# Kernel optimization log

Hardware: AMD Instinct MI355X
Metric: run time of the kernel (lower is better)

Reference implementation:

```python
import jax, jax.numpy as jnp
import numpy as np

B, C, HH, WW = 256, 1024, 7, 7
S = HH * WW            # 49 tokens
D = 1024               # hidden_size
L = 2                  # encoder_layers (nhead arg, swapped in source)
H = 2                  # attention heads (num_layers arg, swapped in source)
HD = D // H            # 512 head dim
FF = 1024              # encoder_ffn_dim
OUT = 1024             # head output
EPS = 1e-5


def setup_inputs() -> dict:
    key = jax.random.key(0)
    ks = jax.random.split(key, 10)
    n = lambda k, shape: jax.random.normal(k, shape, jnp.float32) * 0.02
    return dict(
        x=jax.random.normal(ks[0], (B, C, HH, WW), jnp.float32),
        pos_emb=n(ks[1], (S, D)),
        ln1_s=jnp.ones((L, D), jnp.float32), ln1_b=jnp.zeros((L, D), jnp.float32),
        wq=n(ks[2], (L, D, D)), wk=n(ks[3], (L, D, D)),
        wv=n(ks[4], (L, D, D)), wo=n(ks[5], (L, D, D)),
        ln2_s=jnp.ones((L, D), jnp.float32), ln2_b=jnp.zeros((L, D), jnp.float32),
        w1=n(ks[6], (L, D, FF)), b1=jnp.zeros((L, FF), jnp.float32),
        w2=n(ks[7], (L, FF, D)), b2=jnp.zeros((L, D), jnp.float32),
        lnf_s=jnp.ones((D,), jnp.float32), lnf_b=jnp.zeros((D,), jnp.float32),
        head_w=n(ks[8], (S * D, OUT)), head_b=jnp.zeros((OUT,), jnp.float32),
    )


def _ln(x, s, b):
    m = jnp.mean(x, axis=-1, keepdims=True)
    v = jnp.var(x, axis=-1, keepdims=True)
    return (x - m) * jax.lax.rsqrt(v + EPS) * s + b


def reference(x, pos_emb, ln1_s, ln1_b, wq, wk, wv, wo, ln2_s, ln2_b,
              w1, b1, w2, b2, lnf_s, lnf_b, head_w, head_b):
    b = x.shape[0]
    # flatten HxW then permute -> [B, S, D] token sequence
    h = x.reshape(b, C, S).transpose(0, 2, 1)
    # BigBirdPegasus encoder: learned pos emb added to inputs_embeds (no scaling path)
    h = h + pos_emb[None, :, :]
    scale = 1.0 / jnp.sqrt(jnp.float32(HD))
    for i in range(L):
        # --- self-attention block (pre-LN); seq_len=49 triggers original_full attention ---
        r = h
        hn = _ln(h, ln1_s[i], ln1_b[i])
        q = (hn @ wq[i]).reshape(b, S, H, HD)
        k = (hn @ wk[i]).reshape(b, S, H, HD)
        v = (hn @ wv[i]).reshape(b, S, H, HD)
        scores = jnp.einsum('bqhd,bkhd->bhqk', q, k) * scale
        attn = jax.nn.softmax(scores, axis=-1)
        ctx = jnp.einsum('bhqk,bkhd->bqhd', attn, v).reshape(b, S, D)
        h = r + ctx @ wo[i]
        # --- feed-forward block (pre-LN, gelu_new) ---
        r = h
        hn = _ln(h, ln2_s[i], ln2_b[i])
        hn = jax.nn.gelu(hn @ w1[i] + b1[i], approximate=True)
        h = r + hn @ w2[i] + b2[i]
    # BigBirdPegasus applies layernorm_embedding AFTER the layer stack
    h = _ln(h, lnf_s, lnf_b)
    # flatten + linear + relu head
    out = jax.nn.relu(h.reshape(b, S * D) @ head_w + head_b)
    return out
```

## Files before the change

kernel.cpp:

```cpp
#include <hip/hip_runtime.h>
#include <hip/hip_bf16.h>
#include <stdint.h>

#define Bq 256
#define Sq 49
#define Dq 1024
#define Hq 2
#define HDq 512
#define Mq (Bq*Sq)
#define KHEADq (Sq*Dq)
#define STq 3072

typedef unsigned short u16;
typedef short bf16x8 __attribute__((ext_vector_type(8)));
typedef float f32x4 __attribute__((ext_vector_type(4)));

__device__ inline u16 f2bf(float f){
  union { float f; uint32_t u; } c; c.f = f;
  uint32_t r = c.u + 0x7FFFu + ((c.u >> 16) & 1u);
  return (u16)(r >> 16);
}
__device__ inline float bf2f(u16 h){
  union { uint32_t u; float f; } c; c.u = ((uint32_t)h) << 16;
  return c.f;
}

#define GLOAD_LDS16(gp, lp) \
  __builtin_amdgcn_global_load_lds((__attribute__((address_space(1))) void*)(gp), \
                                   (__attribute__((address_space(3))) void*)(lp), 16, 0, 0)
#define MFMA16(a,b,c) __builtin_amdgcn_mfma_f32_16x16x32_bf16(a,b,c,0,0,0)

__global__ __launch_bounds__(256) void prep_kernel(const float* __restrict__ x,
    const float* __restrict__ pos, u16* __restrict__ h, float2* __restrict__ pstat,
    u16* __restrict__ qkv){
  __shared__ float t[49*129];
  int b = blockIdx.x, c0 = blockIdx.y*128;
  int tid = threadIdx.x, lane = tid & 63, wave = tid >> 6;
  if(b == 0){
    uint4* pz = (uint4*)(qkv + (size_t)Mq*STq + (size_t)blockIdx.y*6144);
    pz[tid] = make_uint4(0,0,0,0);
    pz[256+tid] = make_uint4(0,0,0,0);
    pz[512+tid] = make_uint4(0,0,0,0);
  }
  const float* xb = x + (size_t)b*(Dq*Sq) + (size_t)c0*Sq;
  #pragma unroll
  for(int i=0;i<32;i++){
    int cc = wave + i*4;
    if(lane < Sq) t[lane*129 + cc] = xb[(size_t)cc*Sq + lane];
  }
  __syncthreads();
  #pragma unroll
  for(int p=0;p<25;p++){
    int idx = p*256 + tid;
    int s = idx >> 7, cc = idx & 127;
    if(s < Sq){
      float hv = t[s*129 + cc] + pos[s*Dq + c0 + cc];
      h[((size_t)b*Sq + s)*Dq + c0 + cc] = f2bf(hv);
      t[s*129 + cc] = hv;
    }
  }
  __syncthreads();
  int r = tid >> 2, qd = tid & 3;
  if(r < Sq){
    float S=0.f, Q=0.f;
    for(int cc=qd; cc<128; cc+=4){ float vv = t[r*129+cc]; S+=vv; Q+=vv*vv; }
    S += __shfl_xor(S,1); Q += __shfl_xor(Q,1);
    S += __shfl_xor(S,2); Q += __shfl_xor(Q,2);
    if(qd==0){ float2 pp; pp.x=S; pp.y=Q; pstat[(size_t)blockIdx.y*Mq + b*Sq + r] = pp; }
  }
}

__global__ __launch_bounds__(256) void ln_kernel(const u16* __restrict__ hin,
    const float* __restrict__ sc, const float* __restrict__ bi, u16* __restrict__ outp){
  int wave = threadIdx.x >> 6, lane = threadIdx.x & 63;
  int row = blockIdx.x*4 + wave;
  const u16* p = hin + (size_t)row*Dq + lane*16;
  uint4 t0 = *(const uint4*)p;
  uint4 t1 = *(const uint4*)(p + 8);
  float v[16];
  {
    uint32_t wds[8] = {t0.x,t0.y,t0.z,t0.w,t1.x,t1.y,t1.z,t1.w};
    #pragma unroll
    for(int i=0;i<8;i++){
      v[2*i]   = bf2f((u16)(wds[i] & 0xffff));
      v[2*i+1] = bf2f((u16)(wds[i] >> 16));
    }
  }
  float s=0.f, sq=0.f;
  #pragma unroll
  for(int i=0;i<16;i++){ s += v[i]; sq += v[i]*v[i]; }
  #pragma unroll
  for(int o=32;o>=1;o>>=1){ s += __shfl_xor(s,o); sq += __shfl_xor(sq,o); }
  float mean = s * (1.f/Dq);
  float var  = sq * (1.f/Dq) - mean*mean;
  float rs = rsqrtf(var + 1e-5f);
  int c0 = lane*16;
  uint32_t w[8];
  #pragma unroll
  for(int i=0;i<8;i++){
    u16 lo = f2bf((v[2*i]   - mean)*rs*sc[c0+2*i]   + bi[c0+2*i]);
    u16 hi = f2bf((v[2*i+1] - mean)*rs*sc[c0+2*i+1] + bi[c0+2*i+1]);
    w[i] = (uint32_t)lo | ((uint32_t)hi << 16);
  }
  uint4* ob = (uint4*)(outp + (size_t)row*Dq + c0);
  ob[0] = make_uint4(w[0],w[1],w[2],w[3]);
  ob[1] = make_uint4(w[4],w[5],w[6],w[7]);
}

__global__ void transp_all(const float* __restrict__ wq, const float* __restrict__ wk,
    const float* __restrict__ wv, const float* __restrict__ wo,
    const float* __restrict__ w1, const float* __restrict__ w2,
    const float* __restrict__ ln1s, const float* __restrict__ ln2s, u16* __restrict__ outp){
  __shared__ float t[32][33];
  int slot = blockIdx.z; int l = slot / 6, j = slot - l*6;
  const float* srcs[6] = {wq,wk,wv,wo,w1,w2};
  const float* in = srcs[j] + (size_t)l*Dq*Dq;
  const float* sc = (j<3) ? (ln1s + l*Dq) : (j==4 ? (ln2s + l*Dq) : nullptr);
  u16* o = outp + (size_t)slot*Dq*Dq;
  int k0 = blockIdx.x*32, n0 = blockIdx.y*32;
  int tx = threadIdx.x, ty = threadIdx.y;
  #pragma unroll
  for(int i=0;i<4;i++) t[ty+8*i][tx] = in[(size_t)(k0+ty+8*i)*Dq + n0+tx];
  __syncthreads();
  float sck = sc ? sc[k0+tx] : 1.f;
  #pragma unroll
  for(int i=0;i<4;i++) o[(size_t)(n0+ty+8*i)*Dq + k0+tx] = f2bf(t[tx][ty+8*i] * sck);
}

__global__ __launch_bounds__(256) void uv_all_kernel(const float* __restrict__ wq,
    const float* __restrict__ wk, const float* __restrict__ wv, const float* __restrict__ w1,
    const float* __restrict__ ln1s, const float* __restrict__ ln1b,
    const float* __restrict__ ln2s, const float* __restrict__ ln2b, float* __restrict__ uvbuf){
  __shared__ float2 red[8][32];
  int t = threadIdx.x;
  int colg = blockIdx.x*32 + (t & 31);
  int ks = t >> 5;
  int l = colg >> 12, col = colg & 4095;
  int j = col >> 10, n = col & 1023;
  const float* srcs[4] = {wq, wk, wv, w1};
  const float* src = srcs[j] + (size_t)l*Dq*Dq;
  const float* sc = (j<3 ? ln1s : ln2s) + l*Dq;
  const float* bi = (j<3 ? ln1b : ln2b) + l*Dq;
  float u=0.f, v=0.f;
  for(int k=ks*128;k<ks*128+128;k++){
    float val = src[(size_t)k*Dq + n];
    u += sc[k]*val; v += bi[k]*val;
  }
  float2 pp; pp.x=u; pp.y=v;
  red[ks][t&31] = pp;
  __syncthreads();
  if(t < 32){
    float U=0.f, V=0.f;
    #pragma unroll
    for(int s2=0;s2<8;s2++){ float2 q2 = red[s2][t]; U+=q2.x; V+=q2.y; }
    uvbuf[(size_t)(blockIdx.x*32 + t)*2]   = U;
    uvbuf[(size_t)(blockIdx.x*32 + t)*2+1] = V;
  }
}

template<int EPI>
__global__ __launch_bounds__(512, 2) void gemm_nt2(
    const u16* __restrict__ A, int lda,
    const u16* __restrict__ Bt, int ldb,
    void* __restrict__ Cout, const u16* __restrict__ resid,
    const float* __restrict__ bias, int ldc,
    const float2* __restrict__ pstat_in, int nchunk,
    const float* __restrict__ uvp, float2* __restrict__ pstat_out)
{
  __shared__ u16 lds[65536];
  int tid = threadIdx.x, lane = tid & 63;
  int wave = tid >> 6;
  int wm = wave >> 2, wn = wave & 3;
  int l15 = lane & 15, l4 = lane >> 4;
  int swz = (l15 & 7) << 4;

  int gx = gridDim.x, nwg = gx*gridDim.y;
  int orig = blockIdx.y*gx + blockIdx.x;
  int qq = nwg >> 3, rr = nwg & 7;
  int xcd = orig & 7, idx = orig >> 3;
  int wgid = (xcd < rr ? xcd*(qq+1) : rr*(qq+1) + (xcd-rr)*qq) + idx;
  int bx = wgid % gx, by = wgid / gx;
  int m0 = by*256, n0 = bx*256;

  int srow = tid >> 3, scolb = (tid & 7) * 16;
  int scolx = scolb ^ ((srow & 7) << 4);
  auto stage2 = [&](int d, int kt, int h){
    #pragma unroll
    for(int cc=0; cc<2; cc++){
      int c = 2*h + cc;
      if(c < 4){
        int row = c*64 + srow;
        const u16* src = A + (size_t)(m0+row)*lda + kt*64 + (scolx>>1);
        GLOAD_LDS16(src, &lds[d*16384 + c*4096 + tid*8]);
      } else {
        int c4 = c - 4;
        int row = c4*64 + srow;
        const u16* src = Bt + (size_t)(n0+row)*ldb + kt*64 + (scolx>>1);
        GLOAD_LDS16(src, &lds[32768 + d*16384 + c4*4096 + tid*8]);
      }
    }
  };
  auto rdA = [&](int d, int i, int s)->bf16x8{
    int row = wm*128 + i*16 + l15;
    int byt = row*128 + ((s*64 + l4*16) ^ swz);
    return *(const bf16x8*)((const char*)lds + d*32768 + byt);
  };
  auto rdB = [&](int d, int n, int s)->bf16x8{
    int row = wn*64 + n*16 + l15;
    int byt = row*128 + ((s*64 + l4*16) ^ swz);
    return *(const bf16x8*)((const char*)lds + 65536 + d*32768 + byt);
  };

  f32x4 acc[8][4] = {};

  #pragma unroll
  for(int h=0;h<4;h++) stage2(0, 0, h);

  for(int t=0; t<16; ++t){
    int d = t & 1;
    bf16x8 bfr[4][2];
    if(t < 15){
      stage2(d^1, t+1, 0);
      asm volatile("s_waitcnt vmcnt(2)" ::: "memory");
    } else {
      asm volatile("s_waitcnt vmcnt(0)" ::: "memory");
    }
    __builtin_amdgcn_sched_barrier(0);
    __builtin_amdgcn_s_barrier();
    bfr[0][0]=rdB(d,0,0); bfr[0][1]=rdB(d,0,1);
    bfr[1][0]=rdB(d,1,0); bfr[1][1]=rdB(d,1,1);
    bf16x8 a0s0=rdA(d,0,0), a0s1=rdA(d,0,1), a1s0=rdA(d,1,0), a1s1=rdA(d,1,1);
    __builtin_amdgcn_s_setprio(1);
    acc[0][0]=MFMA16(a0s0,bfr[0][0],acc[0][0]); acc[0][0]=MFMA16(a0s1,bfr[0][1],acc[0][0]);
    acc[0][1]=MFMA16(a0s0,bfr[1][0],acc[0][1]); acc[0][1]=MFMA16(a0s1,bfr[1][1],acc[0][1]);
    acc[1][0]=MFMA16(a1s0,bfr[0][0],acc[1][0]); acc[1][0]=MFMA16(a1s1,bfr[0][1],acc[1][0]);
    acc[1][1]=MFMA16(a1s0,bfr[1][0],acc[1][1]); acc[1][1]=MFMA16(a1s1,bfr[1][1],acc[1][1]);
    __builtin_amdgcn_s_setprio(0);
    __builtin_amdgcn_s_barrier();
    bfr[2][0]=rdB(d,2,0); bfr[2][1]=rdB(d,2,1);
    bfr[3][0]=rdB(d,3,0); bfr[3][1]=rdB(d,3,1);
    if(t < 15) stage2(d^1, t+1, 1);
    __builtin_amdgcn_s_barrier();
    __builtin_amdgcn_s_setprio(1);
    acc[0][2]=MFMA16(a0s0,bfr[2][0],acc[0][2]); acc[0][2]=MFMA16(a0s1,bfr[2][1],acc[0][2]);
    acc[0][3]=MFMA16(a0s0,bfr[3][0],acc[0][3]); acc[0][3]=MFMA16(a0s1,bfr[3][1],acc[0][3]);
    acc[1][2]=MFMA16(a1s0,bfr[2][0],acc[1][2]); acc[1][2]=MFMA16(a1s1,bfr[2][1],acc[1][2]);
    acc[1][3]=MFMA16(a1s0,bfr[3][0],acc[1][3]); acc[1][3]=MFMA16(a1s1,bfr[3][1],acc[1][3]);
    __builtin_amdgcn_s_setprio(0);
    __builtin_amdgcn_s_barrier();
    #pragma unroll
    for(int q=1;q<4;q++){
      bf16x8 c0s0=rdA(d,2*q,0), c0s1=rdA(d,2*q,1), c1s0=rdA(d,2*q+1,0), c1s1=rdA(d,2*q+1,1);
      if(t < 15 && q < 3) stage2(d^1, t+1, q+1);
      __builtin_amdgcn_s_barrier();
      __builtin_amdgcn_s_setprio(1);
      #pragma unroll
      for(int n=0;n<4;n++){
        acc[2*q][n]   = MFMA16(c0s0, bfr[n][0], acc[2*q][n]);
        acc[2*q][n]   = MFMA16(c0s1, bfr[n][1], acc[2*q][n]);
        acc[2*q+1][n] = MFMA16(c1s0, bfr[n][0], acc[2*q+1][n]);
        acc[2*q+1][n] = MFMA16(c1s1, bfr[n][1], acc[2*q+1][n]);
      }
      __builtin_amdgcn_s_setprio(0);
      __builtin_amdgcn_s_barrier();
    }
  }

  if constexpr (EPI == 1){
    float2* statsS = (float2*)((char*)lds + 49152);
    float* slotf = (float*)((char*)lds + wave*4096);
    float bv[4];
    #pragma unroll
    for(int n=0;n<4;n++) bv[n] = bias ? bias[n0 + wn*64 + n*16 + l15] : 0.f;
    #pragma unroll
    for(int i=0;i<8;i++){
      #pragma unroll
      for(int n=0;n<4;n++)
        #pragma unroll
        for(int r=0;r<4;r++)
          slotf[(l4*4+r)*64 + n*16 + l15] = acc[i][n][r] + bv[n];
      #pragma unroll
      for(int st=0;st<2;st++){
        int u = st*64 + lane;
        int row = u >> 3, c8 = (u & 7)*8;
        f32x4 lo = *(const f32x4*)&slotf[row*64 + c8];
        f32x4 hi = *(const f32x4*)&slotf[row*64 + c8 + 4];
        size_t o = (size_t)(m0 + wm*128 + i*16 + row)*ldc + n0 + wn*64 + c8;
        bf16x8 rb = *(const bf16x8*)(resid + o);
        bf16x8 ov; float fs=0.f, fq=0.f;
        #pragma unroll
        for(int j=0;j<4;j++){
          float a_ = lo[j] + bf2f((u16)rb[j]);
          float b_ = hi[j] + bf2f((u16)rb[4+j]);
          ov[j]   = (short)f2bf(a_);
          ov[4+j] = (short)f2bf(b_);
          fs += a_ + b_; fq += a_*a_ + b_*b_;
        }
        *(bf16x8*)((u16*)Cout + o) = ov;
        fs += __shfl_xor(fs,1); fq += __shfl_xor(fq,1);
        fs += __shfl_xor(fs,2); fq += __shfl_xor(fq,2);
        fs += __shfl_xor(fs,4); fq += __shfl_xor(fq,4);
        if((lane&7)==0){
          float2 pp; pp.x=fs; pp.y=fq;
          statsS[(wm*128 + i*16 + st*8 + (lane>>3))*4 + wn] = pp;
        }
      }
    }
    __syncthreads();
    if(tid < 256){
      float S=0.f, Q=0.f;
      #pragma unroll
      for(int w2_=0;w2_<4;w2_++){ float2 pp = statsS[tid*4+w2_]; S+=pp.x; Q+=pp.y; }
      float2 pp; pp.x=S; pp.y=Q;
      pstat_out[(size_t)bx*Mq + m0 + tid] = pp;
    }
  } else {
    float2* lstat = (float2*)((char*)lds + 49152);
    if(tid < 256){
      float S=0.f, Q=0.f;
      for(int c=0;c<nchunk;c++){ float2 pp = pstat_in[(size_t)c*Mq + m0 + tid]; S+=pp.x; Q+=pp.y; }
      float mean = S*(1.f/1024.f);
      float var  = Q*(1.f/1024.f) - mean*mean;
      float2 sm; sm.x = rsqrtf(var + 1e-5f); sm.y = mean;
      lstat[tid] = sm;
    }
    __syncthreads();
    u16* slot = (u16*)((char*)lds + wave*2048);
    float uvv[4][2], bv[4];
    #pragma unroll
    for(int n=0;n<4;n++){
      int ncol = n0 + wn*64 + n*16 + l15;
      float2 uv2 = ((const float2*)uvp)[ncol];
      uvv[n][0] = uv2.x; uvv[n][1] = uv2.y;
      if constexpr (EPI == 2) bv[n] = bias[ncol];
    }
    #pragma unroll
    for(int i=0;i<8;i++){
      #pragma unroll
      for(int n=0;n<4;n++)
        #pragma unroll
        for(int r=0;r<4;r++){
          float2 sm = lstat[wm*128 + i*16 + l4*4 + r];
          float va = sm.x*acc[i][n][r] - sm.x*sm.y*uvv[n][0] + uvv[n][1];
          u16 ov;
          if constexpr (EPI == 0){
            ov = f2bf(va);
          } else {
            float xg = va + bv[n];
            float tg = tanhf(0.79788456080286536f*(xg + 0.044715f*xg*xg*xg));
            ov = f2bf(0.5f*xg*(1.f+tg));
          }
          slot[(l4*4+r)*64 + n*16 + l15] = ov;
        }
      #pragma unroll
      for(int st=0;st<2;st++){
        int u = st*64 + lane;
        int row = u >> 3, c8 = (u & 7)*8;
        bf16x8 v8 = *(const bf16x8*)&slot[row*64 + c8];
        *(bf16x8*)((u16*)Cout + (size_t)(m0 + wm*128 + i*16 + row)*ldc + n0 + wn*64 + c8) = v8;
      }
    }
  }
}

__global__ __launch_bounds__(256) void gemm_head(
    const u16* __restrict__ A, const float* __restrict__ W,
    u16* __restrict__ parts)
{
  __shared__ u16 sA[256*32];
  int tid = threadIdx.x, lane = tid & 63;
  int wave = tid >> 6;
  int wm = wave >> 1, wn = wave & 1;
  int l15 = lane & 15, l4 = lane >> 4;
  int c = blockIdx.x, r = blockIdx.y;
  int nz = (c==0) ? 7 : 6;
  int bx = r / nz;
  if(bx >= 8) return;
  int z = c + 8*(r - bx*nz);
  int n0 = bx*128;
  f32x4 acc[8][4] = {};
  const float* wp = W + ((size_t)z*1024 + (size_t)l4*8)*1024 + n0 + wn*64 + l15;
  for(int kt=0;kt<32;kt++){
    #pragma unroll
    for(int cc=0;cc<4;cc++){
      int s2 = cc*256+tid;
      GLOAD_LDS16(A + (size_t)(s2>>2)*KHEADq + (size_t)z*1024 + kt*32 + (s2&3)*8, &sA[s2*8]);
    }
    bf16x8 bfr[4];
    #pragma unroll
    for(int f=0;f<4;f++){
      float wreg[8];
      #pragma unroll
      for(int jj=0;jj<8;jj++)
        wreg[jj] = wp[(size_t)(kt*32+jj)*1024 + f*16];
      bf16x8 bv;
      #pragma unroll
      for(int jj=0;jj<8;jj++)
        bv[jj] = __builtin_bit_cast(short, __float2bfloat16(wreg[jj]));
      bfr[f] = bv;
    }
    __syncthreads();
    bf16x8 af[8];
    #pragma unroll
    for(int i=0;i<8;i++)
      af[i] = *(const bf16x8*)&sA[(wm*128 + i*16 + l15)*32 + l4*8];
    #pragma unroll
    for(int i=0;i<8;i++)
      #pragma unroll
      for(int j=0;j<4;j++)
        acc[i][j] = MFMA16(af[i], bfr[j], acc[i][j]);
    __syncthreads();
  }
  u16* slot = &sA[wave*2048];
  u16* base = parts + (size_t)z*(Bq*1024);
  #pragma unroll
  for(int i=0;i<8;i++){
    #pragma unroll
    for(int j=0;j<4;j++)
      #pragma unroll
      for(int rr=0;rr<4;rr++)
        slot[(l4*4+rr)*64 + j*16 + l15] = f2bf(acc[i][j][rr]);
    #pragma unroll
    for(int st=0;st<2;st++){
      int u = st*64 + lane;
      int row = u >> 3, c8 = (u & 7)*8;
      bf16x8 v8 = *(const bf16x8*)&slot[row*64 + c8];
      *(bf16x8*)(base + (size_t)(wm*128 + i*16 + row)*1024 + n0 + wn*64 + c8) = v8;
    }
  }
}

__global__ __launch_bounds__(256) void attn_kernel(u16* __restrict__ qkv)
{
  __shared__ float sS[64][65];
  __shared__ u16 sP[64][64];
  int bh = blockIdx.x;
  int b = bh >> 1, h = bh & 1;
  int tid = threadIdx.x, lane = tid & 63, wave = tid >> 6;
  int l15 = lane & 15, l4 = lane >> 4;
  f32x4 zero4 = {0.f,0.f,0.f,0.f};
  bf16x8 zb = {0,0,0,0,0,0,0,0};
  f32x4 acc[4];
  #pragma unroll
  for(int i=0;i<4;i++) acc[i] = zero4;
  int srow = wave*16 + l15;
  const u16* qp = qkv + (size_t)(b*Sq + srow)*STq + h*HDq + l4*8;
  const u16* kbase = qkv + (size_t)b*Sq*STq + Dq + h*HDq + l4*8;
  for(int kt=0;kt<16;kt++){
    bf16x8 aq = (srow < Sq) ? *(const bf16x8*)(qp + kt*32) : zb;
    #pragma unroll
    for(int fn=0;fn<4;fn++){
      int s2 = fn*16 + l15;
      bf16x8 bk = (s2 < Sq) ? *(const bf16x8*)(kbase + (size_t)s2*STq + kt*32) : zb;
      acc[fn] = MFMA16(aq, bk, acc[fn]);
    }
  }
  const float scale = 0.04419417382415922f;
  #pragma unroll
  for(int fn=0;fn<4;fn++)
    #pragma unroll
    for(int r=0;r<4;r++)
      sS[wave*16 + l4*4 + r][fn*16 + l15] = acc[fn][r]*scale;
  __syncthreads();
  {
    int r = tid >> 2, qd = tid & 3;
    float mx = -1e30f;
    for(int j=qd;j<Sq;j+=4) mx = fmaxf(mx, sS[r][j]);
    mx = fmaxf(mx, __shfl_xor(mx,1));
    mx = fmaxf(mx, __shfl_xor(mx,2));
    float sum = 0.f;
    for(int j=qd;j<Sq;j+=4){ float e = __expf(sS[r][j]-mx); sS[r][j]=e; sum+=e; }
    sum += __shfl_xor(sum,1);
    sum += __shfl_xor(sum,2);
    float inv = 1.f/sum;
    for(int j=qd;j<64;j+=4) sP[r][j] = (j<Sq)? f2bf(sS[r][j]*inv) : (u16)0;
  }
  __syncthreads();
  bf16x8 ap[2];
  #pragma unroll
  for(int kt2=0;kt2<2;kt2++)
    ap[kt2] = *(const bf16x8*)&sP[wave*16 + l15][kt2*32 + l4*8];
  const u16* vbp = qkv + (size_t)b*Sq*STq + 2*Dq + h*HDq + l15;
  u16* cb = qkv + (size_t)b*Sq*STq + h*HDq;
  for(int fn=0;fn<32;fn++){
    f32x4 c4 = zero4;
    #pragma unroll
    for(int kt2=0;kt2<2;kt2++){
      const u16* vp = vbp + fn*16 + (size_t)(kt2*32 + l4*8)*STq;
      bf16x8 bv;
      #pragma unroll
      for(int jj=0;jj<8;jj++) bv[jj] = (short)vp[(size_t)jj*STq];
      c4 = MFMA16(ap[kt2], bv, c4);
    }
    #pragma unroll
    for(int r=0;r<4;r++){
      int s = wave*16 + l4*4 + r;
      if(s < Sq) cb[(size_t)s*STq + fn*16 + l15] = f2bf(c4[r]);
    }
  }
}

__global__ __launch_bounds__(256) void head_finalize(const u16* __restrict__ parts,
    const float* __restrict__ hb, float* __restrict__ outp){
  int idx = blockIdx.x*256 + threadIdx.x;
  float s = hb[idx & 1023];
  #pragma unroll
  for(int z=0;z<49;z++) s += bf2f(parts[(size_t)z*(Bq*1024) + idx]);
  outp[idx] = fmaxf(s, 0.f);
}

extern "C" void kernel_launch(void* const* d_in, const int* in_sizes, int n_in,
                              void* d_out, int out_size, void* d_ws, size_t ws_size,
                              hipStream_t stream) {
  (void)in_sizes; (void)n_in; (void)out_size;
  const float* x    = (const float*)d_in[0];
  const float* pos  = (const float*)d_in[1];
  const float* ln1s = (const float*)d_in[2];
  const float* ln1b = (const float*)d_in[3];
  const float* wq   = (const float*)d_in[4];
  const float* wk   = (const float*)d_in[5];
  const float* wv   = (const float*)d_in[6];
  const float* wo   = (const float*)d_in[7];
  const float* ln2s = (const float*)d_in[8];
  const float* ln2b = (const float*)d_in[9];
  const float* w1   = (const float*)d_in[10];
  const float* b1   = (const float*)d_in[11];
  const float* w2   = (const float*)d_in[12];
  const float* b2   = (const float*)d_in[13];
  const float* lnfs = (const float*)d_in[14];
  const float* lnfb = (const float*)d_in[15];
  const float* hw   = (const float*)d_in[16];
  const float* hb   = (const float*)d_in[17];
  float* out = (float*)d_out;

  char* ws = (char*)d_ws;
  size_t off = 0;
  auto carve = [&](size_t n) -> char* { char* p = ws + off; off += (n + 255) & ~(size_t)255; return p; };
  u16*   h     = (u16*)  carve((size_t)Mq*Dq*2);
  u16*   act0  = (u16*)  carve((size_t)Mq*Dq*2);
  u16*   act1  = (u16*)  carve((size_t)Mq*Dq*2);
  u16*   qkv   = (u16*)  carve((size_t)(Mq+16)*STq*2);
  u16*   wT    = (u16*)  carve((size_t)12*Dq*Dq*2);
  float2* pstat= (float2*)carve((size_t)8*Mq*sizeof(float2));
  float* uvbuf = (float*)carve((size_t)2*4096*2*4);
  u16*   parts = qkv;
  if (off > ws_size) return;

  prep_kernel<<<dim3(Bq, 8), 256, 0, stream>>>(x, pos, h, pstat, qkv);
  transp_all<<<dim3(32,32,12), dim3(32,8), 0, stream>>>(wq, wk, wv, wo, w1, w2, ln1s, ln2s, wT);
  uv_all_kernel<<<256, 256, 0, stream>>>(wq, wk, wv, w1, ln1s, ln1b, ln2s, ln2b, uvbuf);

  dim3 gg(4, Mq/256);
  dim3 gq(12, Mq/256);
  for(int l=0;l<2;l++){
    u16* qkvT = wT + (size_t)(l*6+0)*Dq*Dq;
    u16* woT  = wT + (size_t)(l*6+3)*Dq*Dq;
    u16* w1T  = wT + (size_t)(l*6+4)*Dq*Dq;
    u16* w2T  = wT + (size_t)(l*6+5)*Dq*Dq;
    const float* uvq = uvbuf + (size_t)l*8192;
    const float* uv1 = uvbuf + (size_t)l*8192 + 3072*2;

    gemm_nt2<0><<<gq, 512, 0, stream>>>(h, Dq, qkvT, Dq, qkv, nullptr, nullptr, STq,
                                        pstat, (l==0)?8:4, uvq, nullptr);
    attn_kernel<<<Bq*Hq, 256, 0, stream>>>(qkv);
    gemm_nt2<1><<<gg, 512, 0, stream>>>(qkv, STq, woT, Dq, h, h, nullptr, Dq,
                                        nullptr, 0, nullptr, pstat);
    gemm_nt2<2><<<gg, 512, 0, stream>>>(h, Dq, w1T, Dq, act1, nullptr, b1 + l*Dq, Dq,
                                        pstat, 4, uv1, nullptr);
    gemm_nt2<1><<<gg, 512, 0, stream>>>(act1, Dq, w2T, Dq, h, h, b2 + l*Dq, Dq,
                                        nullptr, 0, nullptr, pstat);
  }

  ln_kernel<<<Mq/4, 256, 0, stream>>>(h, lnfs, lnfb, act0);
  gemm_head<<<dim3(8,56), 256, 0, stream>>>(act0, hw, parts);
  head_finalize<<<1024, 256, 0, stream>>>(parts, hb, out);
}
```

Baseline: 692.0 us.

## Double-buffer head GEMM loads and split M into two tiles

```diff
diff --git a/kernel.cpp b/kernel.cpp
--- a/kernel.cpp
+++ b/kernel.cpp
@@ -363,58 +363,83 @@
   }
 }
 
-__global__ __launch_bounds__(256) void gemm_head(
+__global__ __launch_bounds__(256, 3) void gemm_head(
     const u16* __restrict__ A, const float* __restrict__ W,
     u16* __restrict__ parts)
 {
-  __shared__ u16 sA[256*32];
+  __shared__ u16 sA[2][128*32];
   int tid = threadIdx.x, lane = tid & 63;
   int wave = tid >> 6;
   int wm = wave >> 1, wn = wave & 1;
   int l15 = lane & 15, l4 = lane >> 4;
-  int c = blockIdx.x, r = blockIdx.y;
-  int nz = (c==0) ? 7 : 6;
-  int bx = r / nz;
-  if(bx >= 8) return;
-  int z = c + 8*(r - bx*nz);
-  int n0 = bx*128;
-  f32x4 acc[8][4] = {};
+  int bx = blockIdx.x, by = blockIdx.y, z = blockIdx.z;
+  int n0 = bx*128, m0 = by*128;
+  size_t abase = (size_t)m0*KHEADq + (size_t)z*1024;
+  f32x4 acc[4][4] = {};
   const float* wp = W + ((size_t)z*1024 + (size_t)l4*8)*1024 + n0 + wn*64 + l15;
-  for(int kt=0;kt<32;kt++){
-    #pragma unroll
-    for(int cc=0;cc<4;cc++){
-      int s2 = cc*256+tid;
-      GLOAD_LDS16(A + (size_t)(s2>>2)*KHEADq + (size_t)z*1024 + kt*32 + (s2&3)*8, &sA[s2*8]);
-    }
+
+  auto stageA = [&](int d, int kt){
+    #pragma unroll
+    for(int c=0;c<2;c++){
+      int s2 = c*256+tid;
+      GLOAD_LDS16(A + abase + (size_t)(s2>>2)*KHEADq + kt*32 + (s2&3)*8, &sA[d][s2*8]);
+    }
+  };
+  float wA[4][8], wB[4][8];
+  auto loadW = [&](float (&dst)[4][8], int kt){
+    #pragma unroll
+    for(int f=0;f<4;f++)
+      #pragma unroll
+      for(int jj=0;jj<8;jj++)
+        dst[f][jj] = wp[(size_t)(kt*32+jj)*1024 + f*16];
+  };
+  auto compute = [&](int d, float (&wreg)[4][8]){
     bf16x8 bfr[4];
     #pragma unroll
     for(int f=0;f<4;f++){
-      float wreg[8];
+      bf16x8 bv;
       #pragma unroll
       for(int jj=0;jj<8;jj++)
-        wreg[jj] = wp[(size_t)(kt*32+jj)*1024 + f*16];
-      bf16x8 bv;
-      #pragma unroll
-      for(int jj=0;jj<8;jj++)
-        bv[jj] = __builtin_bit_cast(short, __float2bfloat16(wreg[jj]));
+        bv[jj] = __builtin_bit_cast(short, __float2bfloat16(wreg[f][jj]));
       bfr[f] = bv;
     }
-    __syncthreads();
-    bf16x8 af[8];
-    #pragma unroll
-    for(int i=0;i<8;i++)
-      af[i] = *(const bf16x8*)&sA[(wm*128 + i*16 + l15)*32 + l4*8];
-    #pragma unroll
-    for(int i=0;i<8;i++)
+    bf16x8 af[4];
+    #pragma unroll
+    for(int i=0;i<4;i++)
+      af[i] = *(const bf16x8*)&sA[d][(wm*64 + i*16 + l15)*32 + l4*8];
+    #pragma unroll
+    for(int i=0;i<4;i++)
       #pragma unroll
       for(int j=0;j<4;j++)
         acc[i][j] = MFMA16(af[i], bfr[j], acc[i][j]);
-    __syncthreads();
-  }
-  u16* slot = &sA[wave*2048];
+  };
+
+  stageA(0, 0);
+  loadW(wA, 0);
+  for(int k2=0; k2<16; ++k2){
+    int kt = 2*k2;
+    stageA(1, kt+1);
+    loadW(wB, kt+1);
+    asm volatile("s_waitcnt vmcnt(34)" ::: "memory");
+    __builtin_amdgcn_s_barrier();
+    compute(0, wA);
+    __builtin_amdgcn_s_barrier();
+    if(k2 < 15){
+      stageA(0, kt+2);
+      loadW(wA, kt+2);
+      asm volatile("s_waitcnt vmcnt(34)" ::: "memory");
+    } else {
+      asm volatile("s_waitcnt vmcnt(0)" ::: "memory");
+    }
+    __builtin_amdgcn_s_barrier();
+    compute(1, wB);
+    __builtin_amdgcn_s_barrier();
+  }
+
+  u16* slot = &sA[0][wave*1024];
   u16* base = parts + (size_t)z*(Bq*1024);
   #pragma unroll
-  for(int i=0;i<8;i++){
+  for(int i=0;i<4;i++){
     #pragma unroll
     for(int j=0;j<4;j++)
       #pragma unroll
@@ -425,7 +450,7 @@
       int u = st*64 + lane;
       int row = u >> 3, c8 = (u & 7)*8;
       bf16x8 v8 = *(const bf16x8*)&slot[row*64 + c8];
-      *(bf16x8*)(base + (size_t)(wm*128 + i*16 + row)*1024 + n0 + wn*64 + c8) = v8;
+      *(bf16x8*)(base + (size_t)(m0 + wm*64 + i*16 + row)*1024 + n0 + wn*64 + c8) = v8;
     }
   }
 }
@@ -572,6 +597,6 @@
   }
 
   ln_kernel<<<Mq/4, 256, 0, stream>>>(h, lnfs, lnfb, act0);
-  gemm_head<<<dim3(8,56), 256, 0, stream>>>(act0, hw, parts);
+  gemm_head<<<dim3(8,2,49), 256, 0, stream>>>(act0, hw, parts);
   head_finalize<<<1024, 256, 0, stream>>>(parts, hb, out);
 }
```

New measurement: 681.7 us. No clear change (-1.5%).
